# Optimization experiments

Measured on AMD Instinct MI355X. Metric: run time of the kernel, lower is better.

Reference implementation:

```python
import jax, jax.numpy as jnp
import numpy as np

N, E, B = 102400, 1638400, 512
DIN, DH, DG = 64, 100, 20
D2, D3 = 200, 300
DF, R, AH, GH, H1, H2, DOUT = 64, 8, 128, 128, 128, 32, 1
EPS = 1e-5


def _xavier(k, i, o):
    lim = float(np.sqrt(6.0 / (i + o)))
    return jax.random.uniform(k, (i, o), minval=-lim, maxval=lim, dtype=jnp.float32)


def setup_inputs() -> dict:
    key = jax.random.key(0)
    ks = jax.random.split(key, 32)
    inp = {
        'node_feat': jax.random.normal(ks[0], (N, DIN), dtype=jnp.float32),
        'self_feat': jax.random.normal(ks[1], (B, D2), dtype=jnp.float32),
        'x3d': jax.random.normal(ks[2], (B, D3), dtype=jnp.float32),
        'src': jax.random.randint(ks[3], (E,), 0, N, dtype=jnp.int32),
        'dst': jax.random.randint(ks[4], (E,), 0, N, dtype=jnp.int32),
        'graph_id': (jnp.arange(N, dtype=jnp.int32) // (N // B)),
        # GCN params (weights stored (in, out))
        'gc1_w': _xavier(ks[5], DIN, DH), 'gc1_b': jnp.zeros((DH,), jnp.float32),
        'gc2_w': _xavier(ks[6], DH, DG), 'gc2_b': jnp.zeros((DG,), jnp.float32),
        # modality gate MLP
        'gate_w1': _xavier(ks[7], DG + D2 + D3, GH), 'gate_b1': jnp.zeros((GH,), jnp.float32),
        'gate_w2': _xavier(ks[8], GH, 3), 'gate_b2': jnp.zeros((3,), jnp.float32),
        # fusion projections + layernorms
        'pg_w': _xavier(ks[9], DG, DF), 'pg_b': jnp.zeros((DF,), jnp.float32),
        'p2_w': _xavier(ks[10], D2, DF), 'p2_b': jnp.zeros((DF,), jnp.float32),
        'p3_w': _xavier(ks[11], D3, DF), 'p3_b': jnp.zeros((DF,), jnp.float32),
        'lng_g': jnp.ones((DF,), jnp.float32), 'lng_b': jnp.zeros((DF,), jnp.float32),
        'ln2_g': jnp.ones((DF,), jnp.float32), 'ln2_b': jnp.zeros((DF,), jnp.float32),
        'ln3_g': jnp.ones((DF,), jnp.float32), 'ln3_b': jnp.zeros((DF,), jnp.float32),
        # low-rank CP factors
        'U_w': _xavier(ks[12], DF, R * DF),
        'V_w': _xavier(ks[13], DF, R * DF),
        'S_w': _xavier(ks[14], DF, R * DF),
        # rank attention MLP
        'attn_w1': _xavier(ks[15], DG + D2 + D3, AH), 'attn_b1': jnp.zeros((AH,), jnp.float32),
        'attn_w2': _xavier(ks[16], AH, R), 'attn_b2': jnp.zeros((R,), jnp.float32),
        # head MLP + batchnorms (training-mode batch stats)
        'fc1_w': _xavier(ks[17], DF, H1), 'fc1_b': jnp.zeros((H1,), jnp.float32),
        'fc2_w': _xavier(ks[18], H1, H2), 'fc2_b': jnp.zeros((H2,), jnp.float32),
        'fc3_w': _xavier(ks[19], H2, DOUT), 'fc3_b': jnp.zeros((DOUT,), jnp.float32),
        'bn1_g': jnp.ones((H1,), jnp.float32), 'bn1_b': jnp.zeros((H1,), jnp.float32),
        'bn2_g': jnp.ones((H2,), jnp.float32), 'bn2_b': jnp.zeros((H2,), jnp.float32),
    }
    return inp


def _gcn(h, src, dst, w, b):
    n = h.shape[0]
    msg = jax.ops.segment_sum(h[src], dst, num_segments=n)           # gather + scatter-add
    deg = jax.ops.segment_sum(jnp.ones((src.shape[0],), h.dtype), dst, num_segments=n)
    agg = msg / jnp.maximum(deg, 1.0)[:, None]                       # mean over mailbox
    return agg @ w + b


def _ln(x, g, b):
    mu = jnp.mean(x, axis=-1, keepdims=True)
    var = jnp.mean(jnp.square(x - mu), axis=-1, keepdims=True)
    return g * (x - mu) * jax.lax.rsqrt(var + EPS) + b


def _bn(x, g, b):
    mu = jnp.mean(x, axis=0)
    var = jnp.mean(jnp.square(x - mu), axis=0)
    return g * (x - mu) * jax.lax.rsqrt(var + EPS) + b


def reference(node_feat, self_feat, x3d, src, dst, graph_id,
              gc1_w, gc1_b, gc2_w, gc2_b,
              gate_w1, gate_b1, gate_w2, gate_b2,
              pg_w, pg_b, p2_w, p2_b, p3_w, p3_b,
              lng_g, lng_b, ln2_g, ln2_b, ln3_g, ln3_b,
              U_w, V_w, S_w,
              attn_w1, attn_b1, attn_w2, attn_b2,
              fc1_w, fc1_b, fc2_w, fc2_b, fc3_w, fc3_b,
              bn1_g, bn1_b, bn2_g, bn2_b):
    b = self_feat.shape[0]
    # two GCN layers (copy_u + mean reduce + linear), relu
    h = jax.nn.relu(_gcn(node_feat, src, dst, gc1_w, gc1_b))
    h = jax.nn.relu(_gcn(h, src, dst, gc2_w, gc2_b))
    # dgl.mean_nodes: per-graph mean readout
    cnt = jax.ops.segment_sum(jnp.ones((h.shape[0],), h.dtype), graph_id, num_segments=b)
    hg = jax.ops.segment_sum(h, graph_id, num_segments=b) / cnt[:, None]  # (B, DG)
    # modality gate
    cat = jnp.concatenate([hg, self_feat, x3d], axis=-1)
    alpha = jax.nn.softmax(jax.nn.relu(cat @ gate_w1 + gate_b1) @ gate_w2 + gate_b2, axis=-1)
    hg2 = hg * alpha[:, 0:1]
    sf2 = self_feat * alpha[:, 1:2]
    x3d2 = x3d * alpha[:, 2:3]
    # low-rank tri-linear fusion with rank attention (dropout = identity, eval mode)
    gp = jax.nn.relu(_ln(hg2 @ pg_w + pg_b, lng_g, lng_b))
    d2 = jax.nn.relu(_ln(sf2 @ p2_w + p2_b, ln2_g, ln2_b))
    d3 = jax.nn.relu(_ln(x3d2 @ p3_w + p3_b, ln3_g, ln3_b))
    g_r = (gp @ U_w).reshape(b, R, DF)
    d2_r = (d2 @ V_w).reshape(b, R, DF)
    d3_r = (d3 @ S_w).reshape(b, R, DF)
    z_r = g_r * d2_r * d3_r                                          # (B, R, DF)
    cat2 = jnp.concatenate([hg2, sf2, x3d2], axis=-1)
    beta = jax.nn.softmax(jax.nn.relu(cat2 @ attn_w1 + attn_b1) @ attn_w2 + attn_b2, axis=-1)
    z = jnp.sum(z_r * beta[:, :, None], axis=1)                      # (B, DF)
    # head MLP with batchnorm (batch statistics)
    out = jax.nn.relu(_bn(z @ fc1_w + fc1_b, bn1_g, bn1_b))
    out = jax.nn.relu(_bn(out @ fc2_w + fc2_b, bn2_g, bn2_b))
    out = out @ fc3_w + fc3_b
    return out
```

## Files before the change

kernel.cpp:

```cpp
#include <hip/hip_runtime.h>

#define N_NODES 102400
#define N_EDGES 1638400
#define BB 512
#define DIN 64
#define DH 100
#define DG 20
#define D2 200
#define D3 300
#define DF 64
#define RR 8
#define H1 128
#define H2 32
#define NPG (N_NODES / BB)
#define EPSV 1e-5f
#define CAP 48
#define TB6 6
#define NSLICE 8
#define SLICEN (N_NODES / NSLICE)

typedef float v2f __attribute__((ext_vector_type(2)));

__device__ __forceinline__ float wave_sum64(float v) {
#pragma unroll
    for (int m = 32; m >= 1; m >>= 1) v += __shfl_xor(v, m, 64);
    return v;
}

__device__ __forceinline__ unsigned enc4_fp8(float x0, float x1, float x2, float x3) {
    int r = __builtin_amdgcn_cvt_pk_fp8_f32(x0, x1, 0, false);
    r = __builtin_amdgcn_cvt_pk_fp8_f32(x2, x3, r, true);
    return (unsigned)r;
}
__device__ __forceinline__ void dec8_acc(uint2 w, float* a) {
    v2f p0 = __builtin_amdgcn_cvt_pk_f32_fp8((int)w.x, false);
    v2f p1 = __builtin_amdgcn_cvt_pk_f32_fp8((int)w.x, true);
    v2f p2 = __builtin_amdgcn_cvt_pk_f32_fp8((int)w.y, false);
    v2f p3 = __builtin_amdgcn_cvt_pk_f32_fp8((int)w.y, true);
    a[0] += p0.x; a[1] += p0.y; a[2] += p1.x; a[3] += p1.y;
    a[4] += p2.x; a[5] += p2.y; a[6] += p3.x; a[7] += p3.y;
}

__global__ __launch_bounds__(256) void prep(
    const float* __restrict__ nf, unsigned* __restrict__ nfb,
    const int* __restrict__ src, const int* __restrict__ dst,
    int* __restrict__ counts, int* __restrict__ col) {
    int b = blockIdx.x, t = threadIdx.x;
    if (b < 6400) {
        int i = b * 256 + t;
        float4 v = ((const float4*)nf)[i];
        nfb[i] = enc4_fp8(v.x, v.y, v.z, v.w);
    } else {
        int idx = b - 6400;
        int slice = idx & 7;
        int chunk = idx >> 3;
        int e = chunk * 256 + t;
        int d = dst[e];
        if ((d / SLICEN) == slice) {
            int pos = atomicAdd(&counts[d], 1);
            if (pos < CAP) col[d * CAP + pos] = src[e];
        }
    }
}

__global__ __launch_bounds__(512) void gcn1_gather(
    const unsigned* __restrict__ nfb, const int* __restrict__ counts,
    const int* __restrict__ col,
    const float* __restrict__ w1, const float* __restrict__ b1,
    const float* __restrict__ w2, unsigned* __restrict__ tb) {
    __shared__ float s_in[8][DIN];
    __shared__ float s_h[8][DH];
    const uint2* nfb2 = (const uint2*)nfb;
    int t = threadIdx.x;
    int wid = t >> 6, l = t & 63;
    int o = l & 7;
    int g = l >> 3;
    int n0 = blockIdx.x * 8;
    int n = n0 + wid;
    int cnt = counts[n]; if (cnt > CAP) cnt = CAP;
    float a[8];
#pragma unroll
    for (int j = 0; j < 8; j++) a[j] = 0.f;
    int idx = (l < cnt) ? col[n * CAP + l] : 0;
    int nIter = cnt >> 3;
    int m = 0;
    for (; m + 3 < nIter; m += 4) {
        int s0 = __shfl(idx, (m + 0) * 8 + g, 64);
        int s1 = __shfl(idx, (m + 1) * 8 + g, 64);
        int s2 = __shfl(idx, (m + 2) * 8 + g, 64);
        int s3 = __shfl(idx, (m + 3) * 8 + g, 64);
        uint2 v0 = nfb2[(size_t)s0 * 8 + o];
        uint2 v1 = nfb2[(size_t)s1 * 8 + o];
        uint2 v2 = nfb2[(size_t)s2 * 8 + o];
        uint2 v3 = nfb2[(size_t)s3 * 8 + o];
        dec8_acc(v0, a); dec8_acc(v1, a); dec8_acc(v2, a); dec8_acc(v3, a);
    }
    for (; m + 1 < nIter; m += 2) {
        int s0 = __shfl(idx, (m + 0) * 8 + g, 64);
        int s1 = __shfl(idx, (m + 1) * 8 + g, 64);
        uint2 v0 = nfb2[(size_t)s0 * 8 + o];
        uint2 v1 = nfb2[(size_t)s1 * 8 + o];
        dec8_acc(v0, a); dec8_acc(v1, a);
    }
    if (m < nIter) {
        int s0 = __shfl(idx, m * 8 + g, 64);
        uint2 v0 = nfb2[(size_t)s0 * 8 + o];
        dec8_acc(v0, a);
    }
    int base = nIter << 3;
    if (base < cnt) {
        int kt = base + g;
        int kl = (kt < cnt) ? kt : (cnt - 1);
        int s = __shfl(idx, kl, 64);
        if (kt < cnt) {
            uint2 v0 = nfb2[(size_t)s * 8 + o];
            dec8_acc(v0, a);
        }
    }
#pragma unroll
    for (int mm = 8; mm <= 32; mm <<= 1) {
#pragma unroll
        for (int j = 0; j < 8; j++) a[j] += __shfl_xor(a[j], mm, 64);
    }
    if (l < 8) {
        float dv = fmaxf((float)cnt, 1.0f);
#pragma unroll
        for (int j = 0; j < 8; j++) s_in[wid][8 * l + j] = a[j] / dv;
    }
    __syncthreads();
    if (t < 400) {
        int j = t / 100;
        int c = t % 100;
        float bv = b1[c];
        float accA = bv, accB = bv;
        for (int i = 0; i < DIN; i++) {
            float w = w1[i * DH + c];
            accA += s_in[j][i] * w;
            accB += s_in[j + 4][i] * w;
        }
        s_h[j][c] = fmaxf(accA, 0.f);
        s_h[j + 4][c] = fmaxf(accB, 0.f);
    }
    __syncthreads();
    if (t < 8 * TB6) {
        int j = t / TB6, p = t % TB6;
        unsigned pk = 0u;
        if (p < 5) {
            float x[4];
#pragma unroll
            for (int q = 0; q < 4; q++) x[q] = 0.f;
            for (int i = 0; i < DH; i++) {
                float hv = s_h[j][i];
#pragma unroll
                for (int q = 0; q < 4; q++) x[q] += hv * w2[i * DG + 4 * p + q];
            }
            pk = enc4_fp8(x[0], x[1], x[2], x[3]);
        }
        tb[(size_t)(n0 + j) * TB6 + p] = pk;
    }
}

__global__ __launch_bounds__(512) void gcn2_gather(
    const unsigned* __restrict__ tb, const int* __restrict__ counts,
    const int* __restrict__ col,
    const float* __restrict__ b2, float* __restrict__ hg) {
    const uint2* tb2 = (const uint2*)tb;
    int t = threadIdx.x;
    int wid = t >> 6, l = t & 63;
    int o = l & 3;
    int g = l >> 2;
    int n = blockIdx.x * 8 + wid;
    int cnt = counts[n]; if (cnt > CAP) cnt = CAP;
    float a[8];
#pragma unroll
    for (int j = 0; j < 8; j++) a[j] = 0.f;
    int idx = (l < cnt) ? col[n * CAP + l] : 0;
    int nIter = cnt >> 4;
    int m = 0;
    for (; m + 1 < nIter; m += 2) {
        int sA = __shfl(idx, (m + 0) * 16 + g, 64);
        int sB = __shfl(idx, (m + 1) * 16 + g, 64);
        uint2 vA = make_uint2(0u, 0u);
        uint2 vB = make_uint2(0u, 0u);
        if (o < 3) { vA = tb2[(size_t)sA * 3 + o]; vB = tb2[(size_t)sB * 3 + o]; }
        dec8_acc(vA, a); dec8_acc(vB, a);
    }
    if (m < nIter) {
        int s = __shfl(idx, m * 16 + g, 64);
        uint2 v = make_uint2(0u, 0u);
        if (o < 3) v = tb2[(size_t)s * 3 + o];
        dec8_acc(v, a);
    }
    int base = nIter << 4;
    if (base < cnt) {
        int kt = base + g;
        int kl = (kt < cnt) ? kt : (cnt - 1);
        int s = __shfl(idx, kl, 64);
        if (kt < cnt && o < 3) {
            uint2 v = tb2[(size_t)s * 3 + o];
            dec8_acc(v, a);
        }
    }
#pragma unroll
    for (int mm = 4; mm <= 32; mm <<= 1) {
#pragma unroll
        for (int j = 0; j < 8; j++) a[j] += __shfl_xor(a[j], mm, 64);
    }
    __shared__ float red[8][DG];
    if (l < 3) {
        float dv = fmaxf((float)cnt, 1.0f);
#pragma unroll
        for (int j = 0; j < 8; j++) {
            int f = 8 * l + j;
            if (f < DG) red[wid][f] = fmaxf(a[j] / dv + b2[f], 0.f);
        }
    }
    __syncthreads();
    if (t < DG) {
        float s = 0.f;
#pragma unroll
        for (int j = 0; j < 8; j++) s += red[j][t];
        atomicAdd(&hg[(blockIdx.x / 25) * DG + t], s * (1.0f / (float)NPG));
    }
}

__device__ __forceinline__ float ln_relu(float x, float g, float b) {
    float mu = wave_sum64(x) * (1.0f / DF);
    float d = x - mu;
    float var = wave_sum64(d * d) * (1.0f / DF);
    float v = g * d * rsqrtf(var + EPSV) + b;
    return fmaxf(v, 0.f);
}

__global__ __launch_bounds__(512) void row_tail(
    const float* __restrict__ hg, const float* __restrict__ sf, const float* __restrict__ x3,
    const float* __restrict__ gate_w1, const float* __restrict__ gate_b1,
    const float* __restrict__ gate_w2, const float* __restrict__ gate_b2,
    const float* __restrict__ attn_w1, const float* __restrict__ attn_b1,
    const float* __restrict__ attn_w2, const float* __restrict__ attn_b2,
    const float* __restrict__ pg_w, const float* __restrict__ pg_b,
    const float* __restrict__ p2_w, const float* __restrict__ p2_b,
    const float* __restrict__ p3_w, const float* __restrict__ p3_b,
    const float* __restrict__ lng_g, const float* __restrict__ lng_b,
    const float* __restrict__ ln2_g, const float* __restrict__ ln2_b,
    const float* __restrict__ ln3_g, const float* __restrict__ ln3_b,
    const float* __restrict__ U_w, const float* __restrict__ V_w, const float* __restrict__ S_w,
    const float* __restrict__ fc1_w, const float* __restrict__ fc1_b,
    float* __restrict__ y1) {
    int row = blockIdx.x, t = threadIdx.x;
    __shared__ float s_in[DG + D2 + D3];
    __shared__ float s_part[512];
    __shared__ float s_hid[128];
    __shared__ float s_sm[RR];
    __shared__ float s_alpha[3];
    __shared__ float s_beta[RR];
    __shared__ float s_gp[DF], s_d2[DF], s_d3[DF], s_z[DF];

    for (int i = t; i < DG + D2 + D3; i += 512)
        s_in[i] = (i < DG) ? hg[row * DG + i]
                : (i < DG + D2) ? sf[row * D2 + (i - DG)]
                : x3[row * D3 + (i - DG - D2)];
    __syncthreads();

    {
        int ks = t >> 7, col = t & 127;
        int k0 = ks * 130;
        float acc = 0.f;
        for (int i = k0; i < k0 + 130; i++) acc += s_in[i] * gate_w1[i * 128 + col];
        s_part[ks * 128 + col] = acc;
    }
    __syncthreads();
    if (t < 128)
        s_hid[t] = fmaxf(s_part[t] + s_part[128 + t] + s_part[256 + t] + s_part[384 + t]
                         + gate_b1[t], 0.f);
    __syncthreads();
    if (t < 3) {
        float p = gate_b2[t];
        for (int i = 0; i < 128; i++) p += s_hid[i] * gate_w2[i * 3 + t];
        s_sm[t] = p;
    }
    __syncthreads();
    if (t == 0) {
        float mx = fmaxf(s_sm[0], fmaxf(s_sm[1], s_sm[2]));
        float e0 = __expf(s_sm[0] - mx), e1 = __expf(s_sm[1] - mx), e2 = __expf(s_sm[2] - mx);
        float inv = 1.0f / (e0 + e1 + e2);
        s_alpha[0] = e0 * inv; s_alpha[1] = e1 * inv; s_alpha[2] = e2 * inv;
    }
    __syncthreads();
    for (int i = t; i < DG + D2 + D3; i += 512) {
        float sc = (i < DG) ? s_alpha[0] : (i < DG + D2) ? s_alpha[1] : s_alpha[2];
        s_in[i] *= sc;
    }
    __syncthreads();

    {
        int ks = t >> 7, col = t & 127;
        int k0 = ks * 130;
        float acc = 0.f;
        for (int i = k0; i < k0 + 130; i++) acc += s_in[i] * attn_w1[i * 128 + col];
        s_part[ks * 128 + col] = acc;
    }
    __syncthreads();
    if (t < 128)
        s_hid[t] = fmaxf(s_part[t] + s_part[128 + t] + s_part[256 + t] + s_part[384 + t]
                         + attn_b1[t], 0.f);
    __syncthreads();
    if (t < RR) {
        float p = attn_b2[t];
        for (int i = 0; i < 128; i++) p += s_hid[i] * attn_w2[i * RR + t];
        s_sm[t] = p;
    }
    __syncthreads();
    if (t == 0) {
        float mx = -1e30f;
#pragma unroll
        for (int k = 0; k < RR; k++) mx = fmaxf(mx, s_sm[k]);
        float se = 0.f, e[RR];
#pragma unroll
        for (int k = 0; k < RR; k++) { e[k] = __expf(s_sm[k] - mx); se += e[k]; }
        float inv = 1.0f / se;
#pragma unroll
        for (int k = 0; k < RR; k++) s_beta[k] = e[k] * inv;
    }
    __syncthreads();

    float rawg = 0.f, raw2 = 0.f, raw3 = 0.f;
    if (t < DF) {
        rawg = pg_b[t];
        for (int i = 0; i < DG; i++) rawg += s_in[i] * pg_w[i * DF + t];
    }
    {
        int ks = t >> 6, col = t & 63;
        int k0 = ks * 25;
        float acc = 0.f;
        for (int u = 0; u < 25; u++) acc += s_in[DG + k0 + u] * p2_w[(k0 + u) * DF + col];
        s_part[ks * 64 + col] = acc;
    }
    __syncthreads();
    if (t < DF) {
        raw2 = p2_b[t];
#pragma unroll
        for (int r = 0; r < 8; r++) raw2 += s_part[r * 64 + t];
    }
    __syncthreads();
    {
        int ks = t >> 6, col = t & 63;
        int k0 = (ks * 300) >> 3, k1 = ((ks + 1) * 300) >> 3;
        float acc = 0.f;
        for (int i = k0; i < k1; i++) acc += s_in[DG + D2 + i] * p3_w[i * DF + col];
        s_part[ks * 64 + col] = acc;
    }
    __syncthreads();
    if (t < DF) {
        raw3 = p3_b[t];
#pragma unroll
        for (int r = 0; r < 8; r++) raw3 += s_part[r * 64 + t];
        s_gp[t] = ln_relu(rawg, lng_g[t], lng_b[t]);
        s_d2[t] = ln_relu(raw2, ln2_g[t], ln2_b[t]);
        s_d3[t] = ln_relu(raw3, ln3_g[t], ln3_b[t]);
    }
    __syncthreads();

    {
        int r = t >> 6, f = t & 63;
        float gu = 0.f, dv = 0.f, ds = 0.f;
        for (int i = 0; i < DF; i++) {
            gu += s_gp[i] * U_w[i * (RR * DF) + r * DF + f];
            dv += s_d2[i] * V_w[i * (RR * DF) + r * DF + f];
            ds += s_d3[i] * S_w[i * (RR * DF) + r * DF + f];
        }
        s_part[r * 64 + f] = s_beta[r] * gu * dv * ds;
    }
    __syncthreads();
    if (t < DF) {
        float zf = 0.f;
#pragma unroll
        for (int r = 0; r < RR; r++) zf += s_part[r * 64 + t];
        s_z[t] = zf;
    }
    __syncthreads();

    {
        int ks = t >> 7, col = t & 127;
        int k0 = ks * 16;
        float acc = 0.f;
        for (int i = k0; i < k0 + 16; i++) acc += s_z[i] * fc1_w[i * H1 + col];
        s_part[ks * 128 + col] = acc;
    }
    __syncthreads();
    if (t < 128)
        y1[row * H1 + t] = s_part[t] + s_part[128 + t] + s_part[256 + t] + s_part[384 + t]
                           + fc1_b[t];
}

__global__ __launch_bounds__(256) void head2(
    const float* __restrict__ y1,
    const float* __restrict__ bn1_g, const float* __restrict__ bn1_b,
    const float* __restrict__ fc2_w, const float* __restrict__ fc2_b,
    float* __restrict__ y2) {
    int row = blockIdx.x, t = threadIdx.x;
    __shared__ float sp[2][H1], sp2[2][H1];
    int h = t >> 7, c = t & 127;
    float s = 0.f, s2 = 0.f;
#pragma unroll 8
    for (int r = h * 256; r < h * 256 + 256; r++) {
        float v = y1[r * H1 + c];
        s += v; s2 += v * v;
    }
    sp[h][c] = s; sp2[h][c] = s2;
    __syncthreads();
    __shared__ float sh[H1];
    if (t < H1) {
        float S = sp[0][t] + sp[1][t];
        float S2 = sp2[0][t] + sp2[1][t];
        float m = S * (1.0f / BB);
        float ri = rsqrtf(S2 * (1.0f / BB) - m * m + EPSV);
        float v = y1[row * H1 + t];
        sh[t] = fmaxf(bn1_g[t] * (v - m) * ri + bn1_b[t], 0.f);
    }
    __syncthreads();
    if (t < H2) {
        float acc = fc2_b[t];
        for (int i = 0; i < H1; i++) acc += sh[i] * fc2_w[i * H2 + t];
        y2[row * H2 + t] = acc;
    }
}

__global__ __launch_bounds__(256) void head3(
    const float* __restrict__ y2,
    const float* __restrict__ bn2_g, const float* __restrict__ bn2_b,
    const float* __restrict__ fc3_w, const float* __restrict__ fc3_b,
    float* __restrict__ out) {
    int t = threadIdx.x;
    __shared__ float smu[H2], sri[H2];
    if (t < H2) {
        float s = 0.f, s2 = 0.f;
#pragma unroll 8
        for (int r = 0; r < BB; r++) {
            float v = y2[r * H2 + t];
            s += v; s2 += v * v;
        }
        float m = s * (1.0f / BB);
        smu[t] = m;
        sri[t] = rsqrtf(s2 * (1.0f / BB) - m * m + EPSV);
    }
    __syncthreads();
    int row = blockIdx.x * 256 + t;
    float acc = fc3_b[0];
    for (int i = 0; i < H2; i++) {
        float v = y2[row * H2 + i];
        v = bn2_g[i] * (v - smu[i]) * sri[i] + bn2_b[i];
        acc += fmaxf(v, 0.f) * fc3_w[i];
    }
    out[row] = acc;
}

extern "C" void kernel_launch(void* const* d_in, const int* in_sizes, int n_in,
                              void* d_out, int out_size, void* d_ws, size_t ws_size,
                              hipStream_t stream) {
    const float* node_feat = (const float*)d_in[0];
    const float* self_feat = (const float*)d_in[1];
    const float* x3d       = (const float*)d_in[2];
    const int*   src       = (const int*)d_in[3];
    const int*   dst       = (const int*)d_in[4];
    const float* gc1_w = (const float*)d_in[6];
    const float* gc1_b = (const float*)d_in[7];
    const float* gc2_w = (const float*)d_in[8];
    const float* gc2_b = (const float*)d_in[9];
    const float* gate_w1 = (const float*)d_in[10];
    const float* gate_b1 = (const float*)d_in[11];
    const float* gate_w2 = (const float*)d_in[12];
    const float* gate_b2 = (const float*)d_in[13];
    const float* pg_w = (const float*)d_in[14];
    const float* pg_b = (const float*)d_in[15];
    const float* p2_w = (const float*)d_in[16];
    const float* p2_b = (const float*)d_in[17];
    const float* p3_w = (const float*)d_in[18];
    const float* p3_b = (const float*)d_in[19];
    const float* lng_g = (const float*)d_in[20];
    const float* lng_b = (const float*)d_in[21];
    const float* ln2_g = (const float*)d_in[22];
    const float* ln2_b = (const float*)d_in[23];
    const float* ln3_g = (const float*)d_in[24];
    const float* ln3_b = (const float*)d_in[25];
    const float* U_w = (const float*)d_in[26];
    const float* V_w = (const float*)d_in[27];
    const float* S_w = (const float*)d_in[28];
    const float* attn_w1 = (const float*)d_in[29];
    const float* attn_b1 = (const float*)d_in[30];
    const float* attn_w2 = (const float*)d_in[31];
    const float* attn_b2 = (const float*)d_in[32];
    const float* fc1_w = (const float*)d_in[33];
    const float* fc1_b = (const float*)d_in[34];
    const float* fc2_w = (const float*)d_in[35];
    const float* fc2_b = (const float*)d_in[36];
    const float* fc3_w = (const float*)d_in[37];
    const float* fc3_b = (const float*)d_in[38];
    const float* bn1_g = (const float*)d_in[39];
    const float* bn1_b = (const float*)d_in[40];
    const float* bn2_g = (const float*)d_in[41];
    const float* bn2_b = (const float*)d_in[42];

    char* base = (char*)d_ws;
    int* counts  = (int*)base;                       base += sizeof(int) * N_NODES;
    int* col     = (int*)base;                       base += sizeof(int) * (size_t)N_NODES * CAP;
    unsigned* nfb = (unsigned*)base;                 base += sizeof(unsigned) * (size_t)N_NODES * 16;
    unsigned* tb  = (unsigned*)base;                 base += sizeof(unsigned) * (size_t)N_NODES * TB6;
    float* hg    = (float*)base;                     base += sizeof(float) * BB * DG;
    float* y1    = (float*)base;                     base += sizeof(float) * BB * H1;
    float* y2    = (float*)base;                     base += sizeof(float) * BB * H2;
    float* outf  = (float*)d_out;

    hipMemsetAsync(counts, 0, sizeof(int) * N_NODES, stream);
    hipMemsetAsync(hg, 0, sizeof(float) * BB * DG, stream);

    prep<<<6400 + 51200, 256, 0, stream>>>(node_feat, nfb, src, dst, counts, col);

    gcn1_gather<<<N_NODES / 8, 512, 0, stream>>>(nfb, counts, col,
                                                 gc1_w, gc1_b, gc2_w, tb);
    gcn2_gather<<<N_NODES / 8, 512, 0, stream>>>(tb, counts, col, gc2_b, hg);

    row_tail<<<BB, 512, 0, stream>>>(hg, self_feat, x3d,
                                     gate_w1, gate_b1, gate_w2, gate_b2,
                                     attn_w1, attn_b1, attn_w2, attn_b2,
                                     pg_w, pg_b, p2_w, p2_b, p3_w, p3_b,
                                     lng_g, lng_b, ln2_g, ln2_b, ln3_g, ln3_b,
                                     U_w, V_w, S_w, fc1_w, fc1_b, y1);
    head2<<<BB, 256, 0, stream>>>(y1, bn1_g, bn1_b, fc2_w, fc2_b, y2);
    head3<<<BB / 256, 256, 0, stream>>>(y2, bn2_g, bn2_b, fc3_w, fc3_b, outf);
}
```

Measured before the change: 460.4 us.

## Bucket edges by destination slice in LDS before building CSR adjacency

Edge-to-adjacency construction becomes two passes. First, each block reads a chunk of edges once, bins packed (local dst, src) entries per node slice in shared memory, and appends them to per-slice global lists. Then a separate kernel places the entries into per-node columns with slice-local atomics. This replaces the previous scheme, which read every edge eight times (once per slice) to get locality. The cost is an extra kernel, an intermediate buffer, and fixed capacity caps (BINSZ, SLCAP) that could silently drop edges if a slice or bin overflows.

```diff
diff --git a/kernel.cpp b/kernel.cpp
--- a/kernel.cpp
+++ b/kernel.cpp
@@ -18,6 +18,10 @@
 #define TB6 6
 #define NSLICE 8
 #define SLICEN (N_NODES / NSLICE)
+#define EB 4096
+#define NBB (N_EDGES / EB)
+#define BINSZ 768
+#define SLCAP 212992
 
 typedef float v2f __attribute__((ext_vector_type(2)));
 
@@ -44,22 +48,59 @@
 __global__ __launch_bounds__(256) void prep(
     const float* __restrict__ nf, unsigned* __restrict__ nfb,
     const int* __restrict__ src, const int* __restrict__ dst,
-    int* __restrict__ counts, int* __restrict__ col) {
+    int* __restrict__ sliceCnt, unsigned* __restrict__ sliceList) {
     int b = blockIdx.x, t = threadIdx.x;
     if (b < 6400) {
         int i = b * 256 + t;
         float4 v = ((const float4*)nf)[i];
         nfb[i] = enc4_fp8(v.x, v.y, v.z, v.w);
-    } else {
-        int idx = b - 6400;
-        int slice = idx & 7;
-        int chunk = idx >> 3;
-        int e = chunk * 256 + t;
+        return;
+    }
+    __shared__ unsigned bins[NSLICE][BINSZ];
+    __shared__ int bcnt[NSLICE];
+    __shared__ int bbase[NSLICE];
+    if (t < NSLICE) bcnt[t] = 0;
+    __syncthreads();
+    int e0 = (b - 6400) * EB;
+    for (int i = t; i < EB; i += 256) {
+        int e = e0 + i;
         int d = dst[e];
-        if ((d / SLICEN) == slice) {
-            int pos = atomicAdd(&counts[d], 1);
-            if (pos < CAP) col[d * CAP + pos] = src[e];
-        }
+        int slice = d / SLICEN;
+        int pos = atomicAdd(&bcnt[slice], 1);
+        if (pos < BINSZ)
+            bins[slice][pos] = ((unsigned)(d - slice * SLICEN) << 17) | (unsigned)src[e];
+    }
+    __syncthreads();
+    if (t < NSLICE) {
+        int c = bcnt[t]; if (c > BINSZ) c = BINSZ;
+        bcnt[t] = c;
+        bbase[t] = atomicAdd(&sliceCnt[t], c);
+    }
+    __syncthreads();
+    for (int sl = 0; sl < NSLICE; sl++) {
+        int c = bcnt[sl], ba = bbase[sl];
+        for (int i = t; i < c; i += 256) {
+            int pos = ba + i;
+            if (pos < SLCAP) sliceList[(size_t)sl * SLCAP + pos] = bins[sl][i];
+        }
+    }
+}
+
+__global__ __launch_bounds__(256) void place(
+    const unsigned* __restrict__ sliceList, const int* __restrict__ sliceCnt,
+    int* __restrict__ counts, int* __restrict__ col) {
+    int slice = blockIdx.x & 7;
+    int seg = blockIdx.x >> 3;
+    int cnt = sliceCnt[slice]; if (cnt > SLCAP) cnt = SLCAP;
+    int chunk = (cnt + 127) >> 7;
+    int i0 = seg * chunk;
+    int i1 = i0 + chunk; if (i1 > cnt) i1 = cnt;
+    for (int i = i0 + threadIdx.x; i < i1; i += 256) {
+        unsigned ent = sliceList[(size_t)slice * SLCAP + i];
+        int d = slice * SLICEN + (int)(ent >> 17);
+        int s = (int)(ent & 0x1ffffu);
+        int pos = atomicAdd(&counts[d], 1);
+        if (pos < CAP) col[d * CAP + pos] = s;
     }
 }
 
@@ -502,8 +543,10 @@
     const float* bn2_b = (const float*)d_in[42];
 
     char* base = (char*)d_ws;
+    int* sliceCnt = (int*)base;                      base += sizeof(int) * NSLICE;
     int* counts  = (int*)base;                       base += sizeof(int) * N_NODES;
     int* col     = (int*)base;                       base += sizeof(int) * (size_t)N_NODES * CAP;
+    unsigned* sliceList = (unsigned*)base;           base += sizeof(unsigned) * (size_t)NSLICE * SLCAP;
     unsigned* nfb = (unsigned*)base;                 base += sizeof(unsigned) * (size_t)N_NODES * 16;
     unsigned* tb  = (unsigned*)base;                 base += sizeof(unsigned) * (size_t)N_NODES * TB6;
     float* hg    = (float*)base;                     base += sizeof(float) * BB * DG;
@@ -511,10 +554,11 @@
     float* y2    = (float*)base;                     base += sizeof(float) * BB * H2;
     float* outf  = (float*)d_out;
 
-    hipMemsetAsync(counts, 0, sizeof(int) * N_NODES, stream);
+    hipMemsetAsync(sliceCnt, 0, sizeof(int) * (NSLICE + N_NODES), stream);
     hipMemsetAsync(hg, 0, sizeof(float) * BB * DG, stream);
 
-    prep<<<6400 + 51200, 256, 0, stream>>>(node_feat, nfb, src, dst, counts, col);
+    prep<<<6400 + NBB, 256, 0, stream>>>(node_feat, nfb, src, dst, sliceCnt, sliceList);
+    place<<<1024, 256, 0, stream>>>(sliceList, sliceCnt, counts, col);
 
     gcn1_gather<<<N_NODES / 8, 512, 0, stream>>>(nfb, counts, col,
                                                  gc1_w, gc1_b, gc2_w, tb);
```

Result: slower. 477.9 us (+3.8%).
